# Performance work log

Measured on AMD Instinct MI355X. Metric: run time of the kernel, lower is better.

Reference implementation:

```python
import jax, jax.numpy as jnp
import numpy as np

PS = 8; STRIDE = 1; NVALS = 31
DELTA = 0.05; ETA = 0.01; TAU = 0.1
B = 2; CIN = 32; H = 64; W = 64
HP = (H - PS) // STRIDE + 1
WP = (W - PS) // STRIDE + 1
TWO_PI = 2.0 * np.pi

# patch-local coordinate grid (torch.meshgrid 'ij': y varies along rows)
_lin = np.linspace(-1.0, 1.0, PS).astype(np.float32)
YG = jnp.asarray(np.tile(_lin[:, None], (1, PS)))[None, :, :, None, None]  # [1,ps,ps,1,1]
XG = jnp.asarray(np.tile(_lin[None, :], (PS, 1)))[None, :, :, None, None]

ANGLE_RANGE = jnp.asarray(np.linspace(0.0, TWO_PI, NVALS + 1, dtype=np.float32)[:NVALS])
XY_RANGE = jnp.asarray(np.linspace(-3.0, 3.0, NVALS, dtype=np.float32))

# unfold/fold index maps: pixel (hp*stride + px, wp*stride + py)
RI = jnp.arange(PS)[:, None] + STRIDE * jnp.arange(HP)[None, :]  # [ps,hp]
CI = jnp.arange(PS)[:, None] + STRIDE * jnp.arange(WP)[None, :]  # [ps,wp]
R4 = RI[:, None, :, None]  # [ps,1,hp,1]
C4 = CI[None, :, None, :]  # [1,ps,1,wp]


def conv1x1(x, w):
    return jnp.einsum('bchw,oc->bohw', x, w)


def bn(x, gamma, beta, eps=1e-5):
    # BatchNorm2d in training mode: batch statistics, biased variance
    m = x.mean(axis=(0, 2, 3), keepdims=True)
    v = x.var(axis=(0, 2, 3), keepdims=True)
    return gamma[None, :, None, None] * (x - m) * jax.lax.rsqrt(v + eps) + beta[None, :, None, None]


def silu(x):
    return x * jax.nn.sigmoid(x)


def params_to_distances(params):
    # params: [n,5,hp,wp] -> dists [n,2,ps,ps,hp,wp]
    x0 = params[:, 3][:, None, None]  # [n,1,1,hp,wp]
    y0 = params[:, 4][:, None, None]
    ang = jnp.sort(jnp.mod(params[:, :3], TWO_PI), axis=1)
    a1 = ang[:, 0][:, None, None]
    a2 = ang[:, 1][:, None, None]
    a3 = ang[:, 2][:, None, None]
    a4 = 0.5 * (a1 + a3) + jnp.where(jnp.mod(0.5 * (a1 - a3), TWO_PI) >= np.pi, np.pi, 0.0)

    def g(dt):
        return (dt / np.pi - 1.0) ** 35

    def line(a):
        return -jnp.sin(a) * (XG - x0) + jnp.cos(a) * (YG - y0)

    d42 = jnp.mod(a2 - a4, TWO_PI)
    sgn42 = jnp.where(d42 < np.pi, 1.0, -1.0)
    dist42 = sgn42 * jnp.minimum(sgn42 * line(a4), -sgn42 * line(a2)) + g(d42) * TAU
    d13 = jnp.mod(a3 - a1, TWO_PI)
    sgn13 = jnp.where(d13 < np.pi, 1.0, -1.0)
    dist13 = sgn13 * jnp.minimum(sgn13 * line(a1), -sgn13 * line(a3)) + g(d13) * TAU
    return jnp.stack([dist13, dist42], axis=1)


def wedges_of(dists):
    hd = 0.5 * (1.0 + (2.0 / np.pi) * jnp.arctan(dists / ETA))
    h0, h1 = hd[:, 0], hd[:, 1]
    return jnp.stack([1.0 - h0, h0 * (1.0 - h1), h0 * h1], axis=1)  # [n,3,ps,ps,hp,wp]


def dcp(params, imgp):
    # params [n,5,hp,wp], imgp [c,ps,ps,hp,wp]
    dists = params_to_distances(params)
    w = wedges_of(dists)
    wsum = w.sum(axis=(2, 3))  # [n,3,hp,wp]
    cnum = jnp.einsum('cxyHW,nkxyHW->nckHW', imgp, w)
    colors = cnum / (wsum[:, None] + 1e-10)  # [n,c,3,hp,wp]
    patches = jnp.einsum('nkxyHW,nckHW->ncxyHW', w, colors)
    return dists, colors, patches


def boundaries_of(dists):
    d1, d2 = dists[:, 0:1], dists[:, 1:2]
    mad = jnp.where(d1 < 0.0, -d1,
                    jnp.where(d2 < 0.0, jnp.minimum(d1, -d2), jnp.minimum(d1, d2)))
    return 1.0 / (1.0 + (mad / DELTA) ** 2)


def fold(patches):
    # [B,C,ps,ps,hp,wp] -> [B,C,H,W] (sum over overlapping patches)
    Bn, C = patches.shape[:2]
    return jnp.zeros((Bn, C, H, W), patches.dtype).at[:, :, R4, C4].add(patches)


def forward(x, reduce_w, reduce_gamma, reduce_beta, fb_w, fb_gamma, fb_beta, fi_w, fi_gamma, fi_beta):
    xr = silu(bn(conv1x1(x, reduce_w), reduce_gamma, reduce_beta))  # [B,3,H,W]
    imgp = xr[:, :, R4, C4]  # unfold -> [B,3,ps,ps,hp,wp]
    num_patches = jnp.zeros((H, W), xr.dtype).at[R4, C4].add(
        jnp.ones((PS, PS, HP, WP), xr.dtype))

    params = jnp.zeros((x.shape[0], 5, HP, WP), xr.dtype)

    def make_step(i, prange):
        def step(p_b, imgp_b):
            pq = jnp.repeat(p_b[None], NVALS, axis=0)  # [n,5,hp,wp]
            pq = pq.at[:, i].add(prange[:, None, None])
            _, _, patches = dcp(pq, imgp_b)
            loss = ((imgp_b[None] - patches) ** 2).mean(axis=(2, 3)).sum(axis=1)  # [n,hp,wp]
            best = jnp.argmin(loss, axis=0)
            vals = jnp.take_along_axis(pq[:, i], best[None], axis=0)[0]
            return p_b.at[i].set(vals)
        return step

    for i in range(5):  # coordinate descent over 3 angles then x0, y0
        prange = ANGLE_RANGE if i < 3 else XY_RANGE
        params = jax.vmap(make_step(i, prange))(params, imgp)

    def finalize(p_b, imgp_b):
        dists, _, patches = dcp(p_b[None], imgp_b)
        return patches[0], boundaries_of(dists)[0]

    patches_all, lb_all = jax.vmap(finalize)(params, imgp)
    smoothed = fold(patches_all) / num_patches[None, None]  # [B,3,H,W]
    gb = fold(lb_all) / num_patches[None, None]             # [B,1,H,W]
    gb3 = jnp.broadcast_to(gb, (gb.shape[0], 3, H, W))
    boundaries = silu(bn(conv1x1(gb3, fb_w), fb_gamma, fb_beta))
    image = silu(bn(conv1x1(smoothed, fi_w), fi_gamma, fi_beta))
    return boundaries, image


def setup_inputs() -> dict:
    key = jax.random.key(0)
    ks = jax.random.split(key, 4)
    return {
        'x': jax.random.normal(ks[0], (B, CIN, H, W), jnp.float32),
        'reduce_w': jax.random.normal(ks[1], (3, CIN), jnp.float32) * 0.1,
        'reduce_gamma': jnp.ones((3,), jnp.float32),
        'reduce_beta': jnp.zeros((3,), jnp.float32),
        'fb_w': jax.random.normal(ks[2], (1, 3), jnp.float32) * 0.3,
        'fb_gamma': jnp.ones((1,), jnp.float32),
        'fb_beta': jnp.zeros((1,), jnp.float32),
        'fi_w': jax.random.normal(ks[3], (1, 3), jnp.float32) * 0.3,
        'fi_gamma': jnp.ones((1,), jnp.float32),
        'fi_beta': jnp.zeros((1,), jnp.float32),
    }


def reference(x, reduce_w, reduce_gamma, reduce_beta, fb_w, fb_gamma, fb_beta, fi_w, fi_gamma, fi_beta):
    return forward(x, reduce_w, reduce_gamma, reduce_beta, fb_w, fb_gamma, fb_beta, fi_w, fi_gamma, fi_beta)
```

## Files before the change

### kernel.cpp

```cpp
#include <hip/hip_runtime.h>
#include <math.h>

#define B_    2
#define CIN_  32
#define H_    64
#define W_    64
#define HP_   57
#define WP_   57
#define NP_   (B_*HP_*WP_)
#define NVALS_ 31

#define XR_OFF   0
#define PAR_OFF  24576
#define FP_OFF   57066
#define FG_OFF   81642
#define TMPB_OFF 89834
#define TMPI_OFF 98026
#define ST_OFF   106218
#define WS_TOTAL 106228

static __device__ __forceinline__ float mod2pi(float x) {
    const float TP = (float)(2.0 * M_PI);
    float m = fmodf(x, TP);
    return (m < 0.0f) ? (m + TP) : m;
}
static __device__ __forceinline__ float pow35f(float t) {
    float t2 = t * t, t4 = t2 * t2, t8 = t4 * t4, t16 = t8 * t8, t32 = t16 * t16;
    return t32 * t2 * t;
}
static __device__ __forceinline__ float siluf(float x) {
    return x / (1.0f + expf(-x));
}
static __device__ __forceinline__ float wave_sum(float v) {
#pragma unroll
    for (int m = 1; m < 64; m <<= 1) v += __shfl_xor(v, m);
    return v;
}
static __device__ __forceinline__ float lin_of(int k) {
    return (float)(-1.0 + (double)k * (2.0 / 7.0));
}

struct Geo {
    float s1, c1, s2, c2, s3, c3, s4, c4;
    float sgn13, sgn42, g13, g42, x0, y0;
};

static __device__ void setup_geo(float p0, float p1, float p2, float p3, float p4,
                                 Geo& G) {
    const float PIF = (float)M_PI;
    float m0 = mod2pi(p0), m1 = mod2pi(p1), m2 = mod2pi(p2);
    float lo = fminf(m0, m1), hi = fmaxf(m0, m1);
    float a1 = fminf(lo, m2);
    float a3 = fmaxf(hi, m2);
    float a2 = fmaxf(fminf(hi, m2), lo);
    float hm = mod2pi(0.5f * (a1 - a3));
    float a4 = 0.5f * (a1 + a3) + ((hm >= PIF) ? PIF : 0.0f);
    float d42 = mod2pi(a2 - a4);
    G.sgn42 = (d42 < PIF) ? 1.0f : -1.0f;
    G.g42 = pow35f(d42 / PIF - 1.0f) * 0.1f;
    float d13 = mod2pi(a3 - a1);
    G.sgn13 = (d13 < PIF) ? 1.0f : -1.0f;
    G.g13 = pow35f(d13 / PIF - 1.0f) * 0.1f;
    G.s1 = sinf(a1); G.c1 = cosf(a1);
    G.s2 = sinf(a2); G.c2 = cosf(a2);
    G.s3 = sinf(a3); G.c3 = cosf(a3);
    G.s4 = sinf(a4); G.c4 = cosf(a4);
    G.x0 = p3; G.y0 = p4;
}

static __device__ __forceinline__ void dists_at(const Geo& G, float xg, float yg,
                                                float& d13, float& d42) {
    float dx = xg - G.x0, dy = yg - G.y0;
    float l1 = -G.s1 * dx + G.c1 * dy;
    float l2 = -G.s2 * dx + G.c2 * dy;
    float l3 = -G.s3 * dx + G.c3 * dy;
    float l4 = -G.s4 * dx + G.c4 * dy;
    d13 = G.sgn13 * fminf(G.sgn13 * l1, -(G.sgn13 * l3)) + G.g13;
    d42 = G.sgn42 * fminf(G.sgn42 * l4, -(G.sgn42 * l2)) + G.g42;
}

static __device__ __forceinline__ void wedge_at(const Geo& G, float xg, float yg,
                                                float& w0, float& w1, float& w2,
                                                float& d13o, float& d42o) {
    const float C2OPI  = (float)(2.0 / M_PI);
    float d13, d42;
    dists_at(G, xg, yg, d13, d42);
    float hd0 = 0.5f * (1.0f + C2OPI * atanf(d13 * 100.0f));
    float hd1 = 0.5f * (1.0f + C2OPI * atanf(d42 * 100.0f));
    w0 = 1.0f - hd0;
    w1 = hd0 * (1.0f - hd1);
    w2 = hd0 * hd1;
    d13o = d13; d42o = d42;
}

__global__ __launch_bounds__(256) void head_in_conv(const float* __restrict__ x,
                                                    const float* __restrict__ rw,
                                                    float* __restrict__ xr,
                                                    float* __restrict__ st) {
    const int e = blockIdx.x * 256 + threadIdx.x;
    const int b = e >> 12, rem = e & 4095;
    const float* xp = x + (size_t)b * CIN_ * 4096 + rem;
    float a0 = 0.0f, a1 = 0.0f, a2 = 0.0f;
#pragma unroll
    for (int c = 0; c < CIN_; ++c) {
        float xv = xp[c * 4096];
        a0 += rw[c] * xv;
        a1 += rw[32 + c] * xv;
        a2 += rw[64 + c] * xv;
    }
    xr[(b * 3 + 0) * 4096 + rem] = a0;
    xr[(b * 3 + 1) * 4096 + rem] = a1;
    xr[(b * 3 + 2) * 4096 + rem] = a2;
    float s0 = wave_sum(a0), q0 = wave_sum(a0 * a0);
    float s1 = wave_sum(a1), q1 = wave_sum(a1 * a1);
    float s2 = wave_sum(a2), q2 = wave_sum(a2 * a2);
    if ((threadIdx.x & 63) == 0) {
        atomicAdd(&st[0], s0); atomicAdd(&st[1], s1); atomicAdd(&st[2], s2);
        atomicAdd(&st[3], q0); atomicAdd(&st[4], q1); atomicAdd(&st[5], q2);
    }
}

__global__ __launch_bounds__(256) void head_in_apply(const float* __restrict__ gamma,
                                                     const float* __restrict__ beta,
                                                     float* __restrict__ xr,
                                                     const float* __restrict__ st) {
    const int e = blockIdx.x * 256 + threadIdx.x;
    const int b = e >> 12, rem = e & 4095;
#pragma unroll
    for (int o = 0; o < 3; ++o) {
        float mean = st[o] / 8192.0f;
        float var  = st[3 + o] / 8192.0f - mean * mean;
        float sc = gamma[o] / sqrtf(var + 1e-5f);
        float sh = beta[o] - mean * sc;
        int idx = (b * 3 + o) * 4096 + rem;
        xr[idx] = siluf(xr[idx] * sc + sh);
    }
}

__global__ __launch_bounds__(256) void step_kernel(const float* __restrict__ xr,
                                                   float* __restrict__ params,
                                                   int stepIdx) {
    __shared__ float s_img[4][192];
    __shared__ float s_lin[8];
    const int t = threadIdx.x;
    if (t < 8) s_lin[t] = lin_of(t);
    const int lg = t >> 6, lane = t & 63;
    const int patch = blockIdx.x * 4 + lg;
    const bool active = (patch < NP_);
    int b = 0, hp = 0, wp = 0;
    if (active) {
        b = patch / (HP_ * WP_);
        int pi = patch - b * (HP_ * WP_);
        hp = pi / WP_; wp = pi - hp * WP_;
#pragma unroll
        for (int k = 0; k < 3; ++k) {
            int idx = lane + 64 * k;
            int c = idx >> 6, pix = idx & 63;
            s_img[lg][idx] = xr[((b * 3 + c) << 12) + ((hp + (pix >> 3)) << 6) + (wp + (pix & 7))];
        }
    }
    __syncthreads();
    if (!active) return;

    const int cand = lane >> 1;
    const int half = lane & 1;

    const int pbase = ((b * 5) * HP_ + hp) * WP_ + wp;
    const int PSTR = HP_ * WP_;
    float p0 = params[pbase];
    float p1 = params[pbase + PSTR];
    float p2 = params[pbase + 2 * PSTR];
    float p3 = params[pbase + 3 * PSTR];
    float p4 = params[pbase + 4 * PSTR];
    const float base = (stepIdx == 0) ? p0 : (stepIdx == 1) ? p1 :
                       (stepIdx == 2) ? p2 : (stepIdx == 3) ? p3 : p4;
    const int ci = (cand < NVALS_) ? cand : (NVALS_ - 1);
    float add;
    if (stepIdx < 3) add = (float)((double)ci * (6.283185307179586476925286766559 / 31.0));
    else             add = (float)(-3.0 + (double)ci * 0.2);
    const float pv = base + add;
    if (stepIdx == 0) p0 = pv; else if (stepIdx == 1) p1 = pv;
    else if (stepIdx == 2) p2 = pv; else if (stepIdx == 3) p3 = pv; else p4 = pv;

    Geo G; setup_geo(p0, p1, p2, p3, p4, G);

    const float* img = s_img[lg] + half * 32;
    const int yoff = half << 2;

    float ws0 = 0, ws1 = 0;
    float is0 = 0, is1 = 0, is2 = 0;
    float cn00 = 0, cn01 = 0;
    float cn10 = 0, cn11 = 0;
    float cn20 = 0, cn21 = 0;
    float g00 = 0, g01 = 0, g11 = 0;
#pragma unroll
    for (int i = 0; i < 32; ++i) {
        const float xg = s_lin[i & 7];
        const float yg = s_lin[yoff + (i >> 3)];
        float w0, w1, w2, du0, du1;
        wedge_at(G, xg, yg, w0, w1, w2, du0, du1);
        float i0 = img[i], i1 = img[64 + i], i2 = img[128 + i];
        ws0 += w0; ws1 += w1;
        is0 += i0; is1 += i1; is2 += i2;
        cn00 += i0 * w0; cn01 += i0 * w1;
        cn10 += i1 * w0; cn11 += i1 * w1;
        cn20 += i2 * w0; cn21 += i2 * w1;
        g00 += w0 * w0; g01 += w0 * w1; g11 += w1 * w1;
    }
    ws0 += __shfl_xor(ws0, 1); ws1 += __shfl_xor(ws1, 1);
    is0 += __shfl_xor(is0, 1); is1 += __shfl_xor(is1, 1); is2 += __shfl_xor(is2, 1);
    cn00 += __shfl_xor(cn00, 1); cn01 += __shfl_xor(cn01, 1);
    cn10 += __shfl_xor(cn10, 1); cn11 += __shfl_xor(cn11, 1);
    cn20 += __shfl_xor(cn20, 1); cn21 += __shfl_xor(cn21, 1);
    g00 += __shfl_xor(g00, 1); g01 += __shfl_xor(g01, 1); g11 += __shfl_xor(g11, 1);

    float ws2  = 64.0f - ws0 - ws1;
    float cn02 = is0 - cn00 - cn01;
    float cn12 = is1 - cn10 - cn11;
    float cn22 = is2 - cn20 - cn21;
    float g02  = ws0 - g00 - g01;
    float g12  = ws1 - g01 - g11;
    float g22  = ws2 - g02 - g12;

    float r0 = 1.0f / (ws0 + 1e-10f);
    float r1 = 1.0f / (ws1 + 1e-10f);
    float r2 = 1.0f / (ws2 + 1e-10f);
    float c00 = cn00 * r0, c01 = cn01 * r1, c02 = cn02 * r2;
    float c10 = cn10 * r0, c11 = cn11 * r1, c12 = cn12 * r2;
    float c20 = cn20 * r0, c21 = cn21 * r1, c22 = cn22 * r2;

    float loss =
        (c00 * c00 * g00 + c01 * c01 * g11 + c02 * c02 * g22
         + 2.0f * (c00 * c01 * g01 + c00 * c02 * g02 + c01 * c02 * g12)
         - 2.0f * (c00 * cn00 + c01 * cn01 + c02 * cn02))
      + (c10 * c10 * g00 + c11 * c11 * g11 + c12 * c12 * g22
         + 2.0f * (c10 * c11 * g01 + c10 * c12 * g02 + c11 * c12 * g12)
         - 2.0f * (c10 * cn10 + c11 * cn11 + c12 * cn12))
      + (c20 * c20 * g00 + c21 * c21 * g11 + c22 * c22 * g22
         + 2.0f * (c20 * c21 * g01 + c20 * c22 * g02 + c21 * c22 * g12)
         - 2.0f * (c20 * cn20 + c21 * cn21 + c22 * cn22));
    if (cand >= NVALS_) loss = INFINITY;

    float bl = loss; int bi = cand;
#pragma unroll
    for (int off = 32; off > 0; off >>= 1) {
        float ol = __shfl_down(bl, (unsigned)off);
        int   oi = __shfl_down(bi, (unsigned)off);
        if (ol < bl || (ol == bl && oi < bi)) { bl = ol; bi = oi; }
    }
    if (lane == 0) {
        float badd;
        if (stepIdx < 3) badd = (float)((double)bi * (6.283185307179586476925286766559 / 31.0));
        else             badd = (float)(-3.0 + (double)bi * 0.2);
        params[pbase + stepIdx * PSTR] = base + badd;
    }
}

__global__ __launch_bounds__(256) void finalize_kernel(const float* __restrict__ xr,
                                                       const float* __restrict__ params,
                                                       float* __restrict__ foldP,
                                                       float* __restrict__ foldG) {
    __shared__ float s_lin[8];
    if (threadIdx.x < 8) s_lin[threadIdx.x] = lin_of(threadIdx.x);
    __syncthreads();

    const int lane = threadIdx.x & 63;
    const int wave = (blockIdx.x * 256 + threadIdx.x) >> 6;
    if (wave >= NP_) return;
    const int b = wave / (HP_ * WP_);
    int pi = wave - b * (HP_ * WP_);
    const int hp = pi / WP_, wp = pi - hp * WP_;

    const int pbase = ((b * 5) * HP_ + hp) * WP_ + wp;
    const int PSTR = HP_ * WP_;
    Geo G;
    setup_geo(params[pbase], params[pbase + PSTR], params[pbase + 2 * PSTR],
              params[pbase + 3 * PSTR], params[pbase + 4 * PSTR], G);

    const int pr = lane >> 3, pc = lane & 7;
    float xg = s_lin[pc], yg = s_lin[pr];
    float w0, w1, w2, d13, d42;
    wedge_at(G, xg, yg, w0, w1, w2, d13, d42);
    float i0 = xr[((b * 3 + 0) << 12) + ((hp + pr) << 6) + (wp + pc)];
    float i1 = xr[((b * 3 + 1) << 12) + ((hp + pr) << 6) + (wp + pc)];
    float i2 = xr[((b * 3 + 2) << 12) + ((hp + pr) << 6) + (wp + pc)];

    float r[12] = { w0, w1, w2,
                    i0 * w0, i0 * w1, i0 * w2,
                    i1 * w0, i1 * w1, i1 * w2,
                    i2 * w0, i2 * w1, i2 * w2 };
#pragma unroll
    for (int m = 1; m < 64; m <<= 1) {
#pragma unroll
        for (int j = 0; j < 12; ++j) r[j] += __shfl_xor(r[j], m);
    }
    float col[3][3];
#pragma unroll
    for (int c = 0; c < 3; ++c) {
        col[c][0] = r[3 + c * 3 + 0] / (r[0] + 1e-10f);
        col[c][1] = r[3 + c * 3 + 1] / (r[1] + 1e-10f);
        col[c][2] = r[3 + c * 3 + 2] / (r[2] + 1e-10f);
    }
    float o0 = w0 * col[0][0] + w1 * col[0][1] + w2 * col[0][2];
    float o1 = w0 * col[1][0] + w1 * col[1][1] + w2 * col[1][2];
    float o2 = w0 * col[2][0] + w1 * col[2][1] + w2 * col[2][2];

    float mad = (d13 < 0.0f) ? -d13 : ((d42 < 0.0f) ? fminf(d13, -d42) : fminf(d13, d42));
    float tt = mad / 0.05f;
    float lb = 1.0f / (1.0f + tt * tt);

    const int off = ((hp + pr) << 6) + (wp + pc);
    atomicAdd(&foldP[(b * 3 + 0) * 4096 + off], o0);
    atomicAdd(&foldP[(b * 3 + 1) * 4096 + off], o1);
    atomicAdd(&foldP[(b * 3 + 2) * 4096 + off], o2);
    atomicAdd(&foldG[b * 4096 + off], lb);
}

static __device__ __forceinline__ float np_count(int tpos) {
    int lo = (tpos - 56 > 0) ? (tpos - 56) : 0;
    int hi = (tpos < 7) ? tpos : 7;
    return (float)(hi - lo + 1);
}

__global__ __launch_bounds__(256) void head_out_conv(const float* __restrict__ foldP,
                                                     const float* __restrict__ foldG,
                                                     const float* __restrict__ fb_w,
                                                     const float* __restrict__ fi_w,
                                                     float* __restrict__ tmpB,
                                                     float* __restrict__ tmpI,
                                                     float* __restrict__ st) {
    const int e = blockIdx.x * 256 + threadIdx.x;
    const int b = e >> 12, h = (e >> 6) & 63, w = e & 63;
    const float npv = np_count(h) * np_count(w);
    float gv = foldG[e] / npv;
    float vb = fb_w[0] * gv + fb_w[1] * gv + fb_w[2] * gv;
    const int off = (h << 6) + w;
    float s0 = foldP[(b * 3 + 0) * 4096 + off] / npv;
    float s1 = foldP[(b * 3 + 1) * 4096 + off] / npv;
    float s2 = foldP[(b * 3 + 2) * 4096 + off] / npv;
    float vi = fi_w[0] * s0 + fi_w[1] * s1 + fi_w[2] * s2;
    tmpB[e] = vb;
    tmpI[e] = vi;
    float sb = wave_sum(vb), qb = wave_sum(vb * vb);
    float si = wave_sum(vi), qi = wave_sum(vi * vi);
    if ((threadIdx.x & 63) == 0) {
        atomicAdd(&st[6], sb); atomicAdd(&st[7], qb);
        atomicAdd(&st[8], si); atomicAdd(&st[9], qi);
    }
}

__global__ __launch_bounds__(256) void head_out_apply(const float* __restrict__ tmpB,
                                                      const float* __restrict__ tmpI,
                                                      const float* __restrict__ fb_g,
                                                      const float* __restrict__ fb_b,
                                                      const float* __restrict__ fi_g,
                                                      const float* __restrict__ fi_b,
                                                      const float* __restrict__ st,
                                                      float* __restrict__ out) {
    const int e = blockIdx.x * 256 + threadIdx.x;
    {
        float mean = st[6] / 8192.0f;
        float var  = st[7] / 8192.0f - mean * mean;
        float sc = fb_g[0] / sqrtf(var + 1e-5f);
        float sh = fb_b[0] - mean * sc;
        out[e] = siluf(tmpB[e] * sc + sh);
    }
    {
        float mean = st[8] / 8192.0f;
        float var  = st[9] / 8192.0f - mean * mean;
        float sc = fi_g[0] / sqrtf(var + 1e-5f);
        float sh = fi_b[0] - mean * sc;
        out[8192 + e] = siluf(tmpI[e] * sc + sh);
    }
}

extern "C" void kernel_launch(void* const* d_in, const int* in_sizes, int n_in,
                              void* d_out, int out_size, void* d_ws, size_t ws_size,
                              hipStream_t stream) {
    (void)in_sizes; (void)n_in; (void)out_size; (void)ws_size;
    const float* x        = (const float*)d_in[0];
    const float* reduce_w = (const float*)d_in[1];
    const float* reduce_g = (const float*)d_in[2];
    const float* reduce_b = (const float*)d_in[3];
    const float* fb_w     = (const float*)d_in[4];
    const float* fb_g     = (const float*)d_in[5];
    const float* fb_b     = (const float*)d_in[6];
    const float* fi_w     = (const float*)d_in[7];
    const float* fi_g     = (const float*)d_in[8];
    const float* fi_b     = (const float*)d_in[9];
    float* ws     = (float*)d_ws;
    float* xr     = ws + XR_OFF;
    float* params = ws + PAR_OFF;
    float* foldP  = ws + FP_OFF;
    float* foldG  = ws + FG_OFF;
    float* tmpB   = ws + TMPB_OFF;
    float* tmpI   = ws + TMPI_OFF;
    float* st     = ws + ST_OFF;
    float* out    = (float*)d_out;

    hipMemsetAsync(params, 0, (size_t)(WS_TOTAL - PAR_OFF) * sizeof(float), stream);

    head_in_conv<<<32, 256, 0, stream>>>(x, reduce_w, xr, st);
    head_in_apply<<<32, 256, 0, stream>>>(reduce_g, reduce_b, xr, st);
    for (int i = 0; i < 5; ++i)
        step_kernel<<<(NP_ + 3) / 4, 256, 0, stream>>>(xr, params, i);
    finalize_kernel<<<(NP_ + 3) / 4, 256, 0, stream>>>(xr, params, foldP, foldG);
    head_out_conv<<<32, 256, 0, stream>>>(foldP, foldG, fb_w, fi_w, tmpB, tmpI, st);
    head_out_apply<<<32, 256, 0, stream>>>(tmpB, tmpI, fb_g, fb_b, fi_g, fi_b, st, out);
}
```

Before: 283.1 us.

## Fuse BN apply, five search steps and finalize into one per-patch kernel

Merges the head BN/SiLU apply, the five per-parameter candidate-search launches and the finalize/fold kernel into a single kernel. Each wave keeps its patch image in shared memory and its best parameters in registers across all steps. This removes six launches, the params buffer round-trips through global memory, and the repeated patch image loads. It also folds the sign factors into precomputed line coefficients, hoists the row terms out of the inner loop, and changes head_in_conv to 128-thread blocks. The outer step loop is not unrolled, which may add some loop and register overhead.

```diff
diff --git a/kernel.cpp b/kernel.cpp
--- a/kernel.cpp
+++ b/kernel.cpp
@@ -11,13 +11,12 @@
 #define NVALS_ 31
 
 #define XR_OFF   0
-#define PAR_OFF  24576
-#define FP_OFF   57066
-#define FG_OFF   81642
-#define TMPB_OFF 89834
-#define TMPI_OFF 98026
-#define ST_OFF   106218
-#define WS_TOTAL 106228
+#define FP_OFF   24576
+#define FG_OFF   49152
+#define ST_OFF   57344
+#define TMPB_OFF 57360
+#define TMPI_OFF 65552
+#define WS_TOTAL 73744
 
 static __device__ __forceinline__ float mod2pi(float x) {
     const float TP = (float)(2.0 * M_PI);
@@ -41,7 +40,8 @@
 }
 
 struct Geo {
-    float s1, c1, s2, c2, s3, c3, s4, c4;
+    float X1, Y1, X3, Y3;
+    float X4, Y4, X2, Y2;
     float sgn13, sgn42, g13, g42, x0, y0;
 };
 
@@ -61,43 +61,43 @@
     float d13 = mod2pi(a3 - a1);
     G.sgn13 = (d13 < PIF) ? 1.0f : -1.0f;
     G.g13 = pow35f(d13 / PIF - 1.0f) * 0.1f;
-    G.s1 = sinf(a1); G.c1 = cosf(a1);
-    G.s2 = sinf(a2); G.c2 = cosf(a2);
-    G.s3 = sinf(a3); G.c3 = cosf(a3);
-    G.s4 = sinf(a4); G.c4 = cosf(a4);
+    float s1 = sinf(a1), c1 = cosf(a1);
+    float s2 = sinf(a2), c2 = cosf(a2);
+    float s3 = sinf(a3), c3 = cosf(a3);
+    float s4 = sinf(a4), c4 = cosf(a4);
+    G.X1 = -G.sgn13 * s1;  G.Y1 =  G.sgn13 * c1;
+    G.X3 =  G.sgn13 * s3;  G.Y3 = -G.sgn13 * c3;
+    G.X4 = -G.sgn42 * s4;  G.Y4 =  G.sgn42 * c4;
+    G.X2 =  G.sgn42 * s2;  G.Y2 = -G.sgn42 * c2;
     G.x0 = p3; G.y0 = p4;
 }
 
 static __device__ __forceinline__ void dists_at(const Geo& G, float xg, float yg,
                                                 float& d13, float& d42) {
     float dx = xg - G.x0, dy = yg - G.y0;
-    float l1 = -G.s1 * dx + G.c1 * dy;
-    float l2 = -G.s2 * dx + G.c2 * dy;
-    float l3 = -G.s3 * dx + G.c3 * dy;
-    float l4 = -G.s4 * dx + G.c4 * dy;
-    d13 = G.sgn13 * fminf(G.sgn13 * l1, -(G.sgn13 * l3)) + G.g13;
-    d42 = G.sgn42 * fminf(G.sgn42 * l4, -(G.sgn42 * l2)) + G.g42;
-}
-
-static __device__ __forceinline__ void wedge_at(const Geo& G, float xg, float yg,
-                                                float& w0, float& w1, float& w2,
-                                                float& d13o, float& d42o) {
-    const float C2OPI  = (float)(2.0 / M_PI);
-    float d13, d42;
-    dists_at(G, xg, yg, d13, d42);
+    float u1 = G.X1 * dx + G.Y1 * dy;
+    float u3 = G.X3 * dx + G.Y3 * dy;
+    float u4 = G.X4 * dx + G.Y4 * dy;
+    float u2 = G.X2 * dx + G.Y2 * dy;
+    d13 = G.sgn13 * fminf(u1, u3) + G.g13;
+    d42 = G.sgn42 * fminf(u4, u2) + G.g42;
+}
+
+static __device__ __forceinline__ void wedge_of(float d13, float d42,
+                                                float& w0, float& w1, float& w2) {
+    const float C2OPI = (float)(2.0 / M_PI);
     float hd0 = 0.5f * (1.0f + C2OPI * atanf(d13 * 100.0f));
     float hd1 = 0.5f * (1.0f + C2OPI * atanf(d42 * 100.0f));
     w0 = 1.0f - hd0;
     w1 = hd0 * (1.0f - hd1);
     w2 = hd0 * hd1;
-    d13o = d13; d42o = d42;
-}
-
-__global__ __launch_bounds__(256) void head_in_conv(const float* __restrict__ x,
+}
+
+__global__ __launch_bounds__(128) void head_in_conv(const float* __restrict__ x,
                                                     const float* __restrict__ rw,
                                                     float* __restrict__ xr,
                                                     float* __restrict__ st) {
-    const int e = blockIdx.x * 256 + threadIdx.x;
+    const int e = blockIdx.x * 128 + threadIdx.x;
     const int b = e >> 12, rem = e & 4095;
     const float* xp = x + (size_t)b * CIN_ * 4096 + rem;
     float a0 = 0.0f, a1 = 0.0f, a2 = 0.0f;
@@ -120,26 +120,12 @@
     }
 }
 
-__global__ __launch_bounds__(256) void head_in_apply(const float* __restrict__ gamma,
-                                                     const float* __restrict__ beta,
-                                                     float* __restrict__ xr,
-                                                     const float* __restrict__ st) {
-    const int e = blockIdx.x * 256 + threadIdx.x;
-    const int b = e >> 12, rem = e & 4095;
-#pragma unroll
-    for (int o = 0; o < 3; ++o) {
-        float mean = st[o] / 8192.0f;
-        float var  = st[3 + o] / 8192.0f - mean * mean;
-        float sc = gamma[o] / sqrtf(var + 1e-5f);
-        float sh = beta[o] - mean * sc;
-        int idx = (b * 3 + o) * 4096 + rem;
-        xr[idx] = siluf(xr[idx] * sc + sh);
-    }
-}
-
-__global__ __launch_bounds__(256) void step_kernel(const float* __restrict__ xr,
-                                                   float* __restrict__ params,
-                                                   int stepIdx) {
+__global__ __launch_bounds__(256) void mega_kernel(const float* __restrict__ xr,
+                                                   const float* __restrict__ gamma,
+                                                   const float* __restrict__ beta,
+                                                   const float* __restrict__ st,
+                                                   float* __restrict__ foldP,
+                                                   float* __restrict__ foldG) {
     __shared__ float s_img[4][192];
     __shared__ float s_lin[8];
     const int t = threadIdx.x;
@@ -152,11 +138,16 @@
         b = patch / (HP_ * WP_);
         int pi = patch - b * (HP_ * WP_);
         hp = pi / WP_; wp = pi - hp * WP_;
-#pragma unroll
-        for (int k = 0; k < 3; ++k) {
-            int idx = lane + 64 * k;
-            int c = idx >> 6, pix = idx & 63;
-            s_img[lg][idx] = xr[((b * 3 + c) << 12) + ((hp + (pix >> 3)) << 6) + (wp + (pix & 7))];
+        const int pr = lane >> 3, pc = lane & 7;
+        const int goff = ((hp + pr) << 6) + (wp + pc);
+#pragma unroll
+        for (int c = 0; c < 3; ++c) {
+            float mean = st[c] / 8192.0f;
+            float var  = st[3 + c] / 8192.0f - mean * mean;
+            float sc = gamma[c] / sqrtf(var + 1e-5f);
+            float sh = beta[c] - mean * sc;
+            float v  = xr[((b * 3 + c) << 12) + goff];
+            s_img[lg][64 * c + lane] = siluf(v * sc + sh);
         }
     }
     __syncthreads();
@@ -164,156 +155,148 @@
 
     const int cand = lane >> 1;
     const int half = lane & 1;
-
-    const int pbase = ((b * 5) * HP_ + hp) * WP_ + wp;
-    const int PSTR = HP_ * WP_;
-    float p0 = params[pbase];
-    float p1 = params[pbase + PSTR];
-    float p2 = params[pbase + 2 * PSTR];
-    float p3 = params[pbase + 3 * PSTR];
-    float p4 = params[pbase + 4 * PSTR];
-    const float base = (stepIdx == 0) ? p0 : (stepIdx == 1) ? p1 :
-                       (stepIdx == 2) ? p2 : (stepIdx == 3) ? p3 : p4;
-    const int ci = (cand < NVALS_) ? cand : (NVALS_ - 1);
-    float add;
-    if (stepIdx < 3) add = (float)((double)ci * (6.283185307179586476925286766559 / 31.0));
-    else             add = (float)(-3.0 + (double)ci * 0.2);
-    const float pv = base + add;
-    if (stepIdx == 0) p0 = pv; else if (stepIdx == 1) p1 = pv;
-    else if (stepIdx == 2) p2 = pv; else if (stepIdx == 3) p3 = pv; else p4 = pv;
-
-    Geo G; setup_geo(p0, p1, p2, p3, p4, G);
-
     const float* img = s_img[lg] + half * 32;
     const int yoff = half << 2;
 
-    float ws0 = 0, ws1 = 0;
-    float is0 = 0, is1 = 0, is2 = 0;
-    float cn00 = 0, cn01 = 0;
-    float cn10 = 0, cn11 = 0;
-    float cn20 = 0, cn21 = 0;
-    float g00 = 0, g01 = 0, g11 = 0;
-#pragma unroll
-    for (int i = 0; i < 32; ++i) {
-        const float xg = s_lin[i & 7];
-        const float yg = s_lin[yoff + (i >> 3)];
-        float w0, w1, w2, du0, du1;
-        wedge_at(G, xg, yg, w0, w1, w2, du0, du1);
-        float i0 = img[i], i1 = img[64 + i], i2 = img[128 + i];
-        ws0 += w0; ws1 += w1;
-        is0 += i0; is1 += i1; is2 += i2;
-        cn00 += i0 * w0; cn01 += i0 * w1;
-        cn10 += i1 * w0; cn11 += i1 * w1;
-        cn20 += i2 * w0; cn21 += i2 * w1;
-        g00 += w0 * w0; g01 += w0 * w1; g11 += w1 * w1;
-    }
-    ws0 += __shfl_xor(ws0, 1); ws1 += __shfl_xor(ws1, 1);
-    is0 += __shfl_xor(is0, 1); is1 += __shfl_xor(is1, 1); is2 += __shfl_xor(is2, 1);
-    cn00 += __shfl_xor(cn00, 1); cn01 += __shfl_xor(cn01, 1);
-    cn10 += __shfl_xor(cn10, 1); cn11 += __shfl_xor(cn11, 1);
-    cn20 += __shfl_xor(cn20, 1); cn21 += __shfl_xor(cn21, 1);
-    g00 += __shfl_xor(g00, 1); g01 += __shfl_xor(g01, 1); g11 += __shfl_xor(g11, 1);
-
-    float ws2  = 64.0f - ws0 - ws1;
-    float cn02 = is0 - cn00 - cn01;
-    float cn12 = is1 - cn10 - cn11;
-    float cn22 = is2 - cn20 - cn21;
-    float g02  = ws0 - g00 - g01;
-    float g12  = ws1 - g01 - g11;
-    float g22  = ws2 - g02 - g12;
-
-    float r0 = 1.0f / (ws0 + 1e-10f);
-    float r1 = 1.0f / (ws1 + 1e-10f);
-    float r2 = 1.0f / (ws2 + 1e-10f);
-    float c00 = cn00 * r0, c01 = cn01 * r1, c02 = cn02 * r2;
-    float c10 = cn10 * r0, c11 = cn11 * r1, c12 = cn12 * r2;
-    float c20 = cn20 * r0, c21 = cn21 * r1, c22 = cn22 * r2;
-
-    float loss =
-        (c00 * c00 * g00 + c01 * c01 * g11 + c02 * c02 * g22
-         + 2.0f * (c00 * c01 * g01 + c00 * c02 * g02 + c01 * c02 * g12)
-         - 2.0f * (c00 * cn00 + c01 * cn01 + c02 * cn02))
-      + (c10 * c10 * g00 + c11 * c11 * g11 + c12 * c12 * g22
-         + 2.0f * (c10 * c11 * g01 + c10 * c12 * g02 + c11 * c12 * g12)
-         - 2.0f * (c10 * cn10 + c11 * cn11 + c12 * cn12))
-      + (c20 * c20 * g00 + c21 * c21 * g11 + c22 * c22 * g22
-         + 2.0f * (c20 * c21 * g01 + c20 * c22 * g02 + c21 * c22 * g12)
-         - 2.0f * (c20 * cn20 + c21 * cn21 + c22 * cn22));
-    if (cand >= NVALS_) loss = INFINITY;
-
-    float bl = loss; int bi = cand;
-#pragma unroll
-    for (int off = 32; off > 0; off >>= 1) {
-        float ol = __shfl_down(bl, (unsigned)off);
-        int   oi = __shfl_down(bi, (unsigned)off);
-        if (ol < bl || (ol == bl && oi < bi)) { bl = ol; bi = oi; }
-    }
-    if (lane == 0) {
+    float p0 = 0.0f, p1 = 0.0f, p2 = 0.0f, p3 = 0.0f, p4 = 0.0f;
+
+#pragma unroll 1
+    for (int step = 0; step < 5; ++step) {
+        const float base = (step == 0) ? p0 : (step == 1) ? p1 :
+                           (step == 2) ? p2 : (step == 3) ? p3 : p4;
+        const int ci = (cand < NVALS_) ? cand : (NVALS_ - 1);
+        float add;
+        if (step < 3) add = (float)((double)ci * (6.283185307179586476925286766559 / 31.0));
+        else          add = (float)(-3.0 + (double)ci * 0.2);
+        const float pv = base + add;
+        Geo G;
+        setup_geo((step == 0) ? pv : p0, (step == 1) ? pv : p1,
+                  (step == 2) ? pv : p2, (step == 3) ? pv : p3,
+                  (step == 4) ? pv : p4, G);
+
+        float ws0 = 0, ws1 = 0;
+        float is0 = 0, is1 = 0, is2 = 0;
+        float cn00 = 0, cn01 = 0, cn10 = 0, cn11 = 0, cn20 = 0, cn21 = 0;
+        float g00 = 0, g01 = 0, g11 = 0;
+#pragma unroll 1
+        for (int r = 0; r < 4; ++r) {
+            const float yg = s_lin[yoff + r];
+            const float dy = yg - G.y0;
+            const float t1 = G.Y1 * dy, t3 = G.Y3 * dy;
+            const float t4 = G.Y4 * dy, t2 = G.Y2 * dy;
+#pragma unroll
+            for (int cth = 0; cth < 8; ++cth) {
+                const int i = r * 8 + cth;
+                const float dx = s_lin[cth] - G.x0;
+                float u1 = G.X1 * dx + t1;
+                float u3 = G.X3 * dx + t3;
+                float u4 = G.X4 * dx + t4;
+                float u2 = G.X2 * dx + t2;
+                float d13 = G.sgn13 * fminf(u1, u3) + G.g13;
+                float d42 = G.sgn42 * fminf(u4, u2) + G.g42;
+                float w0, w1, w2;
+                wedge_of(d13, d42, w0, w1, w2);
+                float i0 = img[i], i1 = img[64 + i], i2 = img[128 + i];
+                ws0 += w0; ws1 += w1;
+                is0 += i0; is1 += i1; is2 += i2;
+                cn00 += i0 * w0; cn01 += i0 * w1;
+                cn10 += i1 * w0; cn11 += i1 * w1;
+                cn20 += i2 * w0; cn21 += i2 * w1;
+                g00 += w0 * w0; g01 += w0 * w1; g11 += w1 * w1;
+            }
+        }
+        ws0 += __shfl_xor(ws0, 1); ws1 += __shfl_xor(ws1, 1);
+        is0 += __shfl_xor(is0, 1); is1 += __shfl_xor(is1, 1); is2 += __shfl_xor(is2, 1);
+        cn00 += __shfl_xor(cn00, 1); cn01 += __shfl_xor(cn01, 1);
+        cn10 += __shfl_xor(cn10, 1); cn11 += __shfl_xor(cn11, 1);
+        cn20 += __shfl_xor(cn20, 1); cn21 += __shfl_xor(cn21, 1);
+        g00 += __shfl_xor(g00, 1); g01 += __shfl_xor(g01, 1); g11 += __shfl_xor(g11, 1);
+
+        float ws2  = 64.0f - ws0 - ws1;
+        float cn02 = is0 - cn00 - cn01;
+        float cn12 = is1 - cn10 - cn11;
+        float cn22 = is2 - cn20 - cn21;
+        float g02  = ws0 - g00 - g01;
+        float g12  = ws1 - g01 - g11;
+        float g22  = ws2 - g02 - g12;
+
+        float r0 = 1.0f / (ws0 + 1e-10f);
+        float r1 = 1.0f / (ws1 + 1e-10f);
+        float r2 = 1.0f / (ws2 + 1e-10f);
+        float c00 = cn00 * r0, c01 = cn01 * r1, c02 = cn02 * r2;
+        float c10 = cn10 * r0, c11 = cn11 * r1, c12 = cn12 * r2;
+        float c20 = cn20 * r0, c21 = cn21 * r1, c22 = cn22 * r2;
+
+        float loss =
+            (c00 * c00 * g00 + c01 * c01 * g11 + c02 * c02 * g22
+             + 2.0f * (c00 * c01 * g01 + c00 * c02 * g02 + c01 * c02 * g12)
+             - 2.0f * (c00 * cn00 + c01 * cn01 + c02 * cn02))
+          + (c10 * c10 * g00 + c11 * c11 * g11 + c12 * c12 * g22
+             + 2.0f * (c10 * c11 * g01 + c10 * c12 * g02 + c11 * c12 * g12)
+             - 2.0f * (c10 * cn10 + c11 * cn11 + c12 * cn12))
+          + (c20 * c20 * g00 + c21 * c21 * g11 + c22 * c22 * g22
+             + 2.0f * (c20 * c21 * g01 + c20 * c22 * g02 + c21 * c22 * g12)
+             - 2.0f * (c20 * cn20 + c21 * cn21 + c22 * cn22));
+        if (cand >= NVALS_) loss = INFINITY;
+
+        float bl = loss; int bi = cand;
+#pragma unroll
+        for (int off = 32; off > 0; off >>= 1) {
+            float ol = __shfl_down(bl, (unsigned)off);
+            int   oi = __shfl_down(bi, (unsigned)off);
+            if (ol < bl || (ol == bl && oi < bi)) { bl = ol; bi = oi; }
+        }
+        bi = __shfl(bi, 0);
         float badd;
-        if (stepIdx < 3) badd = (float)((double)bi * (6.283185307179586476925286766559 / 31.0));
-        else             badd = (float)(-3.0 + (double)bi * 0.2);
-        params[pbase + stepIdx * PSTR] = base + badd;
-    }
-}
-
-__global__ __launch_bounds__(256) void finalize_kernel(const float* __restrict__ xr,
-                                                       const float* __restrict__ params,
-                                                       float* __restrict__ foldP,
-                                                       float* __restrict__ foldG) {
-    __shared__ float s_lin[8];
-    if (threadIdx.x < 8) s_lin[threadIdx.x] = lin_of(threadIdx.x);
-    __syncthreads();
-
-    const int lane = threadIdx.x & 63;
-    const int wave = (blockIdx.x * 256 + threadIdx.x) >> 6;
-    if (wave >= NP_) return;
-    const int b = wave / (HP_ * WP_);
-    int pi = wave - b * (HP_ * WP_);
-    const int hp = pi / WP_, wp = pi - hp * WP_;
-
-    const int pbase = ((b * 5) * HP_ + hp) * WP_ + wp;
-    const int PSTR = HP_ * WP_;
-    Geo G;
-    setup_geo(params[pbase], params[pbase + PSTR], params[pbase + 2 * PSTR],
-              params[pbase + 3 * PSTR], params[pbase + 4 * PSTR], G);
-
-    const int pr = lane >> 3, pc = lane & 7;
-    float xg = s_lin[pc], yg = s_lin[pr];
-    float w0, w1, w2, d13, d42;
-    wedge_at(G, xg, yg, w0, w1, w2, d13, d42);
-    float i0 = xr[((b * 3 + 0) << 12) + ((hp + pr) << 6) + (wp + pc)];
-    float i1 = xr[((b * 3 + 1) << 12) + ((hp + pr) << 6) + (wp + pc)];
-    float i2 = xr[((b * 3 + 2) << 12) + ((hp + pr) << 6) + (wp + pc)];
-
-    float r[12] = { w0, w1, w2,
-                    i0 * w0, i0 * w1, i0 * w2,
-                    i1 * w0, i1 * w1, i1 * w2,
-                    i2 * w0, i2 * w1, i2 * w2 };
-#pragma unroll
-    for (int m = 1; m < 64; m <<= 1) {
-#pragma unroll
-        for (int j = 0; j < 12; ++j) r[j] += __shfl_xor(r[j], m);
-    }
-    float col[3][3];
-#pragma unroll
-    for (int c = 0; c < 3; ++c) {
-        col[c][0] = r[3 + c * 3 + 0] / (r[0] + 1e-10f);
-        col[c][1] = r[3 + c * 3 + 1] / (r[1] + 1e-10f);
-        col[c][2] = r[3 + c * 3 + 2] / (r[2] + 1e-10f);
-    }
-    float o0 = w0 * col[0][0] + w1 * col[0][1] + w2 * col[0][2];
-    float o1 = w0 * col[1][0] + w1 * col[1][1] + w2 * col[1][2];
-    float o2 = w0 * col[2][0] + w1 * col[2][1] + w2 * col[2][2];
-
-    float mad = (d13 < 0.0f) ? -d13 : ((d42 < 0.0f) ? fminf(d13, -d42) : fminf(d13, d42));
-    float tt = mad / 0.05f;
-    float lb = 1.0f / (1.0f + tt * tt);
-
-    const int off = ((hp + pr) << 6) + (wp + pc);
-    atomicAdd(&foldP[(b * 3 + 0) * 4096 + off], o0);
-    atomicAdd(&foldP[(b * 3 + 1) * 4096 + off], o1);
-    atomicAdd(&foldP[(b * 3 + 2) * 4096 + off], o2);
-    atomicAdd(&foldG[b * 4096 + off], lb);
+        if (step < 3) badd = (float)((double)bi * (6.283185307179586476925286766559 / 31.0));
+        else          badd = (float)(-3.0 + (double)bi * 0.2);
+        const float bv = base + badd;
+        if (step == 0) p0 = bv; else if (step == 1) p1 = bv;
+        else if (step == 2) p2 = bv; else if (step == 3) p3 = bv; else p4 = bv;
+    }
+
+    {
+        Geo G; setup_geo(p0, p1, p2, p3, p4, G);
+        const int pr = lane >> 3, pc = lane & 7;
+        float xg = s_lin[pc], yg = s_lin[pr];
+        float d13, d42;
+        dists_at(G, xg, yg, d13, d42);
+        float w0, w1, w2;
+        wedge_of(d13, d42, w0, w1, w2);
+        float i0 = s_img[lg][lane];
+        float i1 = s_img[lg][64 + lane];
+        float i2 = s_img[lg][128 + lane];
+
+        float r[12] = { w0, w1, w2,
+                        i0 * w0, i0 * w1, i0 * w2,
+                        i1 * w0, i1 * w1, i1 * w2,
+                        i2 * w0, i2 * w1, i2 * w2 };
+#pragma unroll
+        for (int m = 1; m < 64; m <<= 1) {
+#pragma unroll
+            for (int j = 0; j < 12; ++j) r[j] += __shfl_xor(r[j], m);
+        }
+        float col[3][3];
+#pragma unroll
+        for (int c = 0; c < 3; ++c) {
+            col[c][0] = r[3 + c * 3 + 0] / (r[0] + 1e-10f);
+            col[c][1] = r[3 + c * 3 + 1] / (r[1] + 1e-10f);
+            col[c][2] = r[3 + c * 3 + 2] / (r[2] + 1e-10f);
+        }
+        float o0 = w0 * col[0][0] + w1 * col[0][1] + w2 * col[0][2];
+        float o1 = w0 * col[1][0] + w1 * col[1][1] + w2 * col[1][2];
+        float o2 = w0 * col[2][0] + w1 * col[2][1] + w2 * col[2][2];
+
+        float mad = (d13 < 0.0f) ? -d13 : ((d42 < 0.0f) ? fminf(d13, -d42) : fminf(d13, d42));
+        float tt = mad / 0.05f;
+        float lb = 1.0f / (1.0f + tt * tt);
+
+        const int off = ((hp + pr) << 6) + (wp + pc);
+        atomicAdd(&foldP[(b * 3 + 0) * 4096 + off], o0);
+        atomicAdd(&foldP[(b * 3 + 1) * 4096 + off], o1);
+        atomicAdd(&foldP[(b * 3 + 2) * 4096 + off], o2);
+        atomicAdd(&foldG[b * 4096 + off], lb);
+    }
 }
 
 static __device__ __forceinline__ float np_count(int tpos) {
@@ -390,21 +373,18 @@
     const float* fi_b     = (const float*)d_in[9];
     float* ws     = (float*)d_ws;
     float* xr     = ws + XR_OFF;
-    float* params = ws + PAR_OFF;
     float* foldP  = ws + FP_OFF;
     float* foldG  = ws + FG_OFF;
+    float* st     = ws + ST_OFF;
     float* tmpB   = ws + TMPB_OFF;
     float* tmpI   = ws + TMPI_OFF;
-    float* st     = ws + ST_OFF;
     float* out    = (float*)d_out;
 
-    hipMemsetAsync(params, 0, (size_t)(WS_TOTAL - PAR_OFF) * sizeof(float), stream);
-
-    head_in_conv<<<32, 256, 0, stream>>>(x, reduce_w, xr, st);
-    head_in_apply<<<32, 256, 0, stream>>>(reduce_g, reduce_b, xr, st);
-    for (int i = 0; i < 5; ++i)
-        step_kernel<<<(NP_ + 3) / 4, 256, 0, stream>>>(xr, params, i);
-    finalize_kernel<<<(NP_ + 3) / 4, 256, 0, stream>>>(xr, params, foldP, foldG);
+    hipMemsetAsync(foldP, 0, (size_t)(TMPB_OFF - FP_OFF) * sizeof(float), stream);
+
+    head_in_conv<<<64, 128, 0, stream>>>(x, reduce_w, xr, st);
+    mega_kernel<<<(NP_ + 3) / 4, 256, 0, stream>>>(xr, reduce_g, reduce_b, st,
+                                                   foldP, foldG);
     head_out_conv<<<32, 256, 0, stream>>>(foldP, foldG, fb_w, fi_w, tmpB, tmpI, st);
     head_out_apply<<<32, 256, 0, stream>>>(tmpB, tmpI, fb_g, fb_b, fi_g, fi_b, st, out);
 }
```

Result: faster. 244.4 us (-13.7%).
